# Optimization experiments

Hardware: AMD Instinct MI355X
Metric: run time of the kernel (lower is better)

The kernel has to match this reference:

```python
import jax, jax.numpy as jnp
import numpy as np

B, T, D_MODEL, H, W = 2, 3, 32, 256, 256
N_HEADS, N_LEVELS, N_POINTS = 4, 3, 4


def conv2d(x, w, b, padding=1, dilation=1):
    y = jax.lax.conv_general_dilated(
        x, w, window_strides=(1, 1),
        padding=[(padding, padding), (padding, padding)],
        rhs_dilation=(dilation, dilation),
        dimension_numbers=('NCHW', 'OIHW', 'NCHW'))
    return y + b[None, :, None, None]


def lrelu(x):
    return jnp.where(x >= 0, x, 0.1 * x)


def bilinear_sample(img, x, y):
    # img: (N,C,H,W); x,y: (N,H',W') pixel coords; zero padding outside (grid_sample zeros)
    N, C, Hh, Ww = img.shape
    x0 = jnp.floor(x); y0 = jnp.floor(y)
    lx = x - x0; ly = y - y0
    imf = img.reshape(N, C, Hh * Ww)
    out = jnp.zeros((N, C) + x.shape[1:], img.dtype)
    for dy, dx, wgt in ((0, 0, (1 - lx) * (1 - ly)), (0, 1, lx * (1 - ly)),
                        (1, 0, (1 - lx) * ly), (1, 1, lx * ly)):
        xi = x0 + dx; yi = y0 + dy
        valid = (xi >= 0) & (xi < Ww) & (yi >= 0) & (yi < Hh)
        idx = (jnp.clip(yi, 0, Hh - 1) * Ww + jnp.clip(xi, 0, Ww - 1)).astype(jnp.int32)
        g = jnp.take_along_axis(imf, idx.reshape(N, 1, -1), axis=2).reshape((N, C) + x.shape[1:])
        out = out + g * (wgt * valid)[:, None]
    return out


def flow_warp(x, flow):
    # torch flow_warp with align_corners=True == sampling at pixel coords grid+flow
    N, C, Hh, Ww = x.shape
    gy, gx = jnp.meshgrid(jnp.arange(Hh, dtype=x.dtype), jnp.arange(Ww, dtype=x.dtype), indexing='ij')
    return bilinear_sample(x, gx[None] + flow[:, 0], gy[None] + flow[:, 1])


def ms_deform_attn(value, sampling_locations, attention_weights, h, w):
    # value: (N, L*h*w, Hh, d); loc: (N, Lq, Hh, L, P, 2) in [0,1]; weights: (N, Lq, Hh, L, P)
    # Matches MSDA CUDA kernel: sample at loc*(W,H)-0.5, bilinear, zero pad outside.
    N, _, Hh, d = value.shape
    Lq = sampling_locations.shape[1]
    L, P = sampling_locations.shape[3], sampling_locations.shape[4]
    out = jnp.zeros((N, Lq, Hh, d), value.dtype)
    for l in range(L):
        v = value[:, l * h * w:(l + 1) * h * w].transpose(0, 2, 1, 3)  # (N,Hh,hw,d)
        loc = sampling_locations[:, :, :, l]  # (N,Lq,Hh,P,2)
        x = loc[..., 0] * w - 0.5
        y = loc[..., 1] * h - 0.5
        x0 = jnp.floor(x); y0 = jnp.floor(y)
        lx = x - x0; ly = y - y0
        samp = jnp.zeros((N, Lq, Hh, P, d), value.dtype)
        for dy, dx, wgt in ((0, 0, (1 - lx) * (1 - ly)), (0, 1, lx * (1 - ly)),
                            (1, 0, (1 - lx) * ly), (1, 1, lx * ly)):
            xi = x0 + dx; yi = y0 + dy
            valid = (xi >= 0) & (xi < w) & (yi >= 0) & (yi < h)
            idx = (jnp.clip(yi, 0, h - 1) * w + jnp.clip(xi, 0, w - 1)).astype(jnp.int32)
            idx = idx.transpose(0, 2, 1, 3).reshape(N, Hh, Lq * P)
            g = jnp.take_along_axis(v, idx[..., None], axis=2)  # (N,Hh,Lq*P,d)
            g = g.reshape(N, Hh, Lq, P, d).transpose(0, 2, 1, 3, 4)
            samp = samp + g * (wgt * valid)[..., None]
        out = out + (samp * attention_weights[:, :, :, l][..., None]).sum(axis=3)
    return out.reshape(N, Lq, Hh * d)


def setup_inputs() -> dict:
    key = jax.random.key(0)
    ks = jax.random.split(key, 24)
    def rn(k, shape, s=1.0):
        return jax.random.normal(k, shape, dtype=jnp.float32) * s
    c = D_MODEL
    nofp = N_HEADS * N_LEVELS * N_POINTS
    return {
        'frame': rn(ks[0], (B, T, c, H, W)),
        'srcframe': rn(ks[1], (B, T, c, H, W)),
        'flow_forward': rn(ks[2], (B, T - 1, 2, H, W), 2.0),
        'flow_backward': rn(ks[3], (B, T - 1, 2, H, W), 2.0),
        'W_qk': rn(ks[4], (3 * c, 3 * c + 4, 3, 3), 0.05), 'b_qk': rn(ks[5], (3 * c,), 0.05),
        'W_v': rn(ks[6], (3 * c, 3 * c, 3, 3), 0.05), 'b_v': rn(ks[7], (3 * c,), 0.05),
        'W_vp': rn(ks[8], (c, c, 3, 3), 0.05), 'b_vp': rn(ks[9], (c,), 0.05),
        'W_off': rn(ks[10], (nofp * 2, 3 * c, 3, 3), 0.01), 'b_off': rn(ks[11], (nofp * 2,), 0.5),
        'W_aw': rn(ks[12], (nofp, 3 * c, 3, 3), 0.05), 'b_aw': rn(ks[13], (nofp,), 0.05),
        'W_out': rn(ks[14], (c, c, 3, 3), 0.05), 'b_out': rn(ks[15], (c,), 0.05),
        'W_ffd': rn(ks[16], (c, c, 3, 3), 0.05), 'b_ffd': rn(ks[17], (c,), 0.05),
        'W_ff1': rn(ks[18], (c, 2 * c, 3, 3), 0.05), 'b_ff1': rn(ks[19], (c,), 0.05),
        'W_ff2': rn(ks[20], (c, c, 3, 3), 0.05), 'b_ff2': rn(ks[21], (c,), 0.05),
        'W_fu': rn(ks[22], (c, c, 1, 1), 0.05), 'b_fu': rn(ks[23], (c,), 0.05),
    }


def reference(frame, srcframe, flow_forward, flow_backward,
              W_qk, b_qk, W_v, b_v, W_vp, b_vp, W_off, b_off, W_aw, b_aw,
              W_out, b_out, W_ffd, b_ffd, W_ff1, b_ff1, W_ff2, b_ff2, W_fu, b_fu):
    b, t, c, h, w = frame.shape
    Hh, L, P = N_HEADS, N_LEVELS, N_POINTS
    d = c // Hh
    # flow-warped neighbor frames + flows -> query embedding
    warp01 = flow_warp(frame[:, 0], flow_backward[:, 0])
    warp21 = flow_warp(frame[:, 2], flow_forward[:, 1])
    qk_in = jnp.concatenate([warp01, frame[:, 1], warp21,
                             flow_forward[:, 1], flow_backward[:, 0]], axis=1)
    qureys = lrelu(conv2d(qk_in, W_qk, b_qk))                       # (b, 3c, h, w)
    value = conv2d(frame.reshape(b, t * c, h, w), W_v, b_v)         # (b, 3c, h, w)
    # --- MSDeformAttn_Fusion ---
    val = conv2d(value.reshape(b * t, c, h, w), W_vp, b_vp).reshape(b, t, c, h, w)
    off = conv2d(qureys, W_off, b_off)                               # (b, Hh*L*P*2, h, w)
    aw = conv2d(qureys, W_aw, b_aw)                                  # (b, Hh*L*P, h, w)
    value_flat = val.reshape(b, t, c, h * w).transpose(0, 1, 3, 2).reshape(b, t * h * w, Hh, d)
    off = off.reshape(b, -1, h * w).transpose(0, 2, 1).reshape(b, h * w, Hh, L, P, 2)
    aw = aw.reshape(b, -1, h * w).transpose(0, 2, 1).reshape(b, h * w, Hh, L * P)
    aw = jax.nn.softmax(aw, axis=-1).reshape(b, h * w, Hh, L, P)
    # reference points: pixel centers normalized (masks all zero -> valid_ratios == 1)
    gy, gx = jnp.meshgrid((jnp.arange(h, dtype=off.dtype) + 0.5) / h,
                          (jnp.arange(w, dtype=off.dtype) + 0.5) / w, indexing='ij')
    ref = jnp.stack([gx.reshape(-1), gy.reshape(-1)], -1)            # (hw, 2) (x, y)
    normalizer = jnp.array([w, h], dtype=off.dtype)                  # same for all levels
    loc = ref[None, :, None, None, None, :] + off / normalizer
    attn_out = ms_deform_attn(value_flat, loc, aw, h, w)             # (b, hw, c)
    out = attn_out.reshape(b, h, w, c).transpose(0, 3, 1, 2)
    out = conv2d(out, W_out, b_out)                                  # output_proj
    # --- post-attention ---
    out = conv2d(out, W_ffd, b_ffd) + frame[:, 1]
    tseq = jnp.concatenate([out, srcframe[:, 1]], axis=1)            # (b, 2c, h, w)
    ff = conv2d(lrelu(conv2d(tseq, W_ff1, b_ff1, padding=2, dilation=2)), W_ff2, b_ff2)
    out = out + ff
    out = lrelu(conv2d(out, W_fu, b_fu, padding=0))                  # fusion 1x1
    return out
```

## Files before the change

### kernel.cpp

```cpp
#include <hip/hip_runtime.h>
#include <hip/hip_bf16.h>

typedef __hip_bfloat16 bf16;
typedef unsigned short us;
typedef __attribute__((ext_vector_type(8))) short short8;
typedef __attribute__((ext_vector_type(8))) unsigned short ushortx8;
typedef __attribute__((ext_vector_type(4))) float f32x4;

#define HW 65536
#define IMW 256
#define IMH 256

static __device__ __forceinline__ float u2f(us u) {
  return __uint_as_float(((unsigned)u) << 16);
}
static __device__ __forceinline__ us f2bu(float x) {
  bf16 h = __float2bfloat16(x);
  return *reinterpret_cast<us*>(&h);
}
static __device__ __forceinline__ unsigned pk2(float a, float b) {
  return (unsigned)f2bu(a) | ((unsigned)f2bu(b) << 16);
}

struct PrepArgs {
  const float* src[9];
  us* dst[9];
  int OC[9], CIN[9], KPAD[9];
};

__global__ __launch_bounds__(256) void prep_weights(PrepArgs a) {
  int j = blockIdx.y;
  int n = blockIdx.x * 256 + threadIdx.x;
  int OC = a.OC[j], CIN = a.CIN[j], KPAD = a.KPAD[j];
  int tot = 9 * OC * KPAD;
  if (n >= tot) return;
  int t = n / (OC * KPAD);
  int rem = n - t * OC * KPAD;
  int oc = rem / KPAD;
  int k = rem - oc * KPAD;
  float v = (k < CIN) ? a.src[j][(size_t)(oc * CIN + k) * 9 + t] : 0.f;
  a.dst[j][n] = f2bu(v);
}

__global__ __launch_bounds__(256) void frame_to_nhwc(const float* __restrict__ frame,
                                                     unsigned* __restrict__ fn) {
  int pix = blockIdx.x * 256 + threadIdx.x;
  int b = blockIdx.y;
  const float* s = frame + (size_t)b * 96 * HW + pix;
  unsigned u[48];
#pragma unroll
  for (int j = 0; j < 48; ++j)
    u[j] = pk2(s[(size_t)(2 * j) * HW], s[(size_t)(2 * j + 1) * HW]);
  unsigned* d = fn + ((size_t)b * HW + pix) * 48;
#pragma unroll
  for (int j = 0; j < 12; ++j) {
    uint4 w;
    w.x = u[4 * j]; w.y = u[4 * j + 1]; w.z = u[4 * j + 2]; w.w = u[4 * j + 3];
    *(uint4*)&d[4 * j] = w;
  }
}

static __device__ void warp_nhwc(const us* __restrict__ fn, size_t bbase, int coff,
                                 float x, float y, unsigned* uo) {
  float x0f = floorf(x), y0f = floorf(y);
  float lx = x - x0f, ly = y - y0f;
  int x0 = (int)x0f, y0 = (int)y0f;
  float wt[4] = {(1.f - lx) * (1.f - ly), lx * (1.f - ly), (1.f - lx) * ly, lx * ly};
  float acc[32] = {};
#pragma unroll
  for (int k = 0; k < 4; ++k) {
    int xi = x0 + (k & 1), yi = y0 + (k >> 1);
    if ((unsigned)xi < IMW && (unsigned)yi < IMH) {
      const ushortx8* s =
          (const ushortx8*)(fn + (bbase + (size_t)yi * IMW + xi) * 96 + coff);
      float w = wt[k];
#pragma unroll
      for (int cj = 0; cj < 4; ++cj) {
        ushortx8 vv = s[cj];
#pragma unroll
        for (int e = 0; e < 8; ++e)
          acc[cj * 8 + e] = fmaf(w, u2f(vv[e]), acc[cj * 8 + e]);
      }
    }
  }
#pragma unroll
  for (int j = 0; j < 16; ++j) uo[j] = pk2(acc[2 * j], acc[2 * j + 1]);
}

__global__ __launch_bounds__(256) void build_qkin(
    const us* __restrict__ fn, const float* __restrict__ flowf,
    const float* __restrict__ flowb, unsigned* __restrict__ qk) {
  int pix = blockIdx.x * 256 + threadIdx.x;
  int b = blockIdx.y;
  int px = pix & 255, py = pix >> 8;

  float fbx = flowb[((size_t)(b * 2 + 0) * 2 + 0) * HW + pix];
  float fby = flowb[((size_t)(b * 2 + 0) * 2 + 1) * HW + pix];
  float ffx = flowf[((size_t)(b * 2 + 1) * 2 + 0) * HW + pix];
  float ffy = flowf[((size_t)(b * 2 + 1) * 2 + 1) * HW + pix];

  unsigned u[50];
  {
    const unsigned* s = (const unsigned*)(fn + ((size_t)b * HW + pix) * 96);
#pragma unroll
    for (int j = 0; j < 16; ++j) u[16 + j] = s[16 + j];
  }
  u[48] = pk2(ffx, ffy);
  u[49] = pk2(fbx, fby);

  warp_nhwc(fn, (size_t)b * HW, 0, (float)px + fbx, (float)py + fby, &u[0]);
  warp_nhwc(fn, (size_t)b * HW, 64, (float)px + ffx, (float)py + ffy, &u[32]);

  unsigned* qb = qk + ((size_t)b * HW + pix) * 50;
#pragma unroll
  for (int j = 0; j < 25; ++j) {
    uint2 t;
    t.x = u[2 * j];
    t.y = u[2 * j + 1];
    *(uint2*)(qb + 2 * j) = t;
  }
}

template <int CIN, int CST, int KPAD, int KCH, int DIL, int G, int ZDIV, int CSUB,
          int RES, int OUTMODE, bool LRELU>
__global__ __launch_bounds__(256) void conv3x3_mfma(
    const us* __restrict__ in, const us* __restrict__ W2,
    const float* __restrict__ bias, void* __restrict__ out, int out_cst,
    int out_coff, float* __restrict__ outB, const float* __restrict__ res,
    int res_cst, int res_coff) {
  constexpr int OC = G * 16;
  constexpr int COLS = 16 + 2 * DIL;
  constexpr int ROWS = 8 + 2 * DIL;
  constexpr int HALO = ROWS * COLS;
  constexpr int CIPAD = KCH + 8;
  constexpr int CH = KCH / 8;
  constexpr int NST = KPAD / KCH;
  constexpr int GW0 = (G + 1) / 2;
  __shared__ alignas(16) short lds[HALO * CIPAD];

  const int z = blockIdx.z;
  const int bin = z / ZDIV;
  const int coff = (z % ZDIV) * CSUB;
  const int px0 = blockIdx.x * 16, py0 = blockIdx.y * 8;
  const int lane = threadIdx.x & 63;
  const int wv = threadIdx.x >> 6;
  const int m = lane & 15, q = lane >> 4;
  const int gh = wv & 1, rh = wv >> 1;
  const int goff = gh * GW0;

  f32x4 acc[GW0][4];
#pragma unroll
  for (int g = 0; g < GW0; ++g)
#pragma unroll
    for (int r = 0; r < 4; ++r) acc[g][r] = 0.f;

#pragma unroll 1
  for (int s = 0; s < NST; ++s) {
    for (int c = threadIdx.x; c < HALO * CH; c += 256) {
      int p = c / CH, cb = c - p * CH;
      int row = p / COLS, col = p - row * COLS;
      int gy = py0 + row - DIL, gx = px0 + col - DIL;
      bool ok = ((unsigned)gy < IMH) && ((unsigned)gx < IMW);
      int ci0 = s * KCH + cb * 8;
      const us* gp = in + ((size_t)bin * HW + (size_t)gy * IMW + gx) * CST + coff + ci0;
      if (CIN == KPAD) {
        short8 v = (short8)0;
        if (ok) v = *(const short8*)gp;
        *(short8*)&lds[p * CIPAD + cb * 8] = v;
      } else {
        uint2 h0; h0.x = 0; h0.y = 0;
        uint2 h1; h1.x = 0; h1.y = 0;
        if (ok && ci0 + 4 <= CIN) h0 = *(const uint2*)gp;
        if (ok && ci0 + 8 <= CIN) h1 = *(const uint2*)(gp + 4);
        *(uint2*)&lds[p * CIPAD + cb * 8] = h0;
        *(uint2*)&lds[p * CIPAD + cb * 8 + 4] = h1;
      }
    }
    __syncthreads();

#pragma unroll
    for (int t = 0; t < 9; ++t) {
      const int dy = t / 3 - 1, dx = t - (t / 3) * 3 - 1;
#pragma unroll
      for (int kc = 0; kc < KCH / 32; ++kc) {
        short8 bfr[4];
#pragma unroll
        for (int r = 0; r < 4; ++r) {
          int rr = rh * 4 + r + DIL + dy * DIL;
          int cc = m + DIL + dx * DIL;
          bfr[r] = *(const short8*)&lds[(rr * COLS + cc) * CIPAD + kc * 32 + q * 8];
        }
#pragma unroll
        for (int g = 0; g < GW0; ++g) {
          if (goff + g < G) {
            short8 af = *(const short8*)(W2 +
                (size_t)(t * OC + (goff + g) * 16 + m) * KPAD + s * KCH + kc * 32 + q * 8);
#pragma unroll
            for (int r = 0; r < 4; ++r)
              acc[g][r] =
                  __builtin_amdgcn_mfma_f32_16x16x32_bf16(af, bfr[r], acc[g][r], 0, 0, 0);
          }
        }
      }
    }
    if (s + 1 < NST) __syncthreads();
  }

#pragma unroll
  for (int g = 0; g < GW0; ++g) {
    if (goff + g < G) {
      int oc0 = (goff + g) * 16 + q * 4;
      f32x4 bb = *(const f32x4*)&bias[oc0];
#pragma unroll
      for (int r = 0; r < 4; ++r) {
        int py = py0 + rh * 4 + r;
        int px = px0 + m;
        size_t pix = (size_t)py * IMW + px;
        f32x4 v;
#pragma unroll
        for (int e = 0; e < 4; ++e) {
          float x = acc[g][r][e] + bb[e];
          if (LRELU) x = x >= 0.f ? x : 0.1f * x;
          v[e] = x;
        }
        if (RES == 1) {
          f32x4 rv = *(const f32x4*)&res[((size_t)z * HW + pix) * res_cst + oc0];
#pragma unroll
          for (int e = 0; e < 4; ++e) v[e] += rv[e];
        }
        if (RES == 2) {
#pragma unroll
          for (int e = 0; e < 4; ++e)
            v[e] += res[((size_t)z * res_cst + res_coff + oc0 + e) * HW + pix];
        }
        if (OUTMODE == 0 || OUTMODE == 3) {
          uint2 w;
          w.x = pk2(v[0], v[1]);
          w.y = pk2(v[2], v[3]);
          *(uint2*)&((us*)out)[((size_t)z * HW + pix) * out_cst + out_coff + oc0] = w;
        }
        if (OUTMODE == 2)
          *(f32x4*)&((float*)out)[((size_t)z * HW + pix) * out_cst + oc0] = v;
        if (OUTMODE == 3)
          *(f32x4*)&outB[((size_t)z * HW + pix) * 32 + oc0] = v;
      }
    }
  }
}

__global__ __launch_bounds__(256) void deform_attn(
    const us* __restrict__ valp, const us* __restrict__ off,
    const float* __restrict__ aw, us* __restrict__ outp) {
  int tid = threadIdx.x;
  int hh = tid & 3;
  int pix = blockIdx.x * 64 + (tid >> 2);
  int b = blockIdx.y;
  int px = pix & (IMW - 1), py = pix >> 8;
  float refx = ((float)px + 0.5f) * (1.0f / IMW);
  float refy = ((float)py + 0.5f) * (1.0f / IMH);

  ushortx8 o8[3];
  {
    const ushortx8* ob =
        (const ushortx8*)(off + ((size_t)b * HW + pix) * 96 + hh * 24);
#pragma unroll
    for (int j = 0; j < 3; ++j) o8[j] = ob[j];
  }
  f32x4 a4[3];
  {
    const f32x4* ab = (const f32x4*)(aw + ((size_t)b * HW + pix) * 48 + hh * 12);
#pragma unroll
    for (int j = 0; j < 3; ++j) a4[j] = ab[j];
  }

  float wv[12];
  float mx = -1e30f;
#pragma unroll
  for (int lp = 0; lp < 12; ++lp) {
    wv[lp] = a4[lp >> 2][lp & 3];
    mx = fmaxf(mx, wv[lp]);
  }
  float s = 0.f;
#pragma unroll
  for (int lp = 0; lp < 12; ++lp) {
    wv[lp] = __expf(wv[lp] - mx);
    s += wv[lp];
  }
  float inv = 1.f / s;

  float acc[8] = {0.f, 0.f, 0.f, 0.f, 0.f, 0.f, 0.f, 0.f};
#pragma unroll 1
  for (int l = 0; l < 3; ++l) {
    const us* vbase = valp + ((size_t)(b * 3 + l) * HW) * 32 + hh * 8;
#pragma unroll
    for (int p = 0; p < 4; ++p) {
      int ch = l * 8 + p * 2;
      float ox = u2f(o8[ch >> 3][ch & 7]);
      float oy = u2f(o8[(ch + 1) >> 3][(ch + 1) & 7]);
      float x = (refx + ox * (1.0f / IMW)) * (float)IMW - 0.5f;
      float y = (refy + oy * (1.0f / IMH)) * (float)IMH - 0.5f;
      float x0f = floorf(x), y0f = floorf(y);
      float lx = x - x0f, ly = y - y0f;
      int x0 = (int)x0f, y0 = (int)y0f;
      float a = wv[l * 4 + p] * inv;
      float cw[4] = {(1.f - lx) * (1.f - ly) * a, lx * (1.f - ly) * a,
                     (1.f - lx) * ly * a, lx * ly * a};
#pragma unroll
      for (int k = 0; k < 4; ++k) {
        int xi = x0 + (k & 1), yi = y0 + (k >> 1);
        if ((unsigned)xi < IMW && (unsigned)yi < IMH) {
          const ushortx8 u = *(const ushortx8*)(vbase + (size_t)(yi * IMW + xi) * 32);
          float wgt = cw[k];
#pragma unroll
          for (int dd = 0; dd < 8; ++dd) acc[dd] = fmaf(wgt, u2f(u[dd]), acc[dd]);
        }
      }
    }
  }
  ushortx8 sv;
#pragma unroll
  for (int dd = 0; dd < 8; ++dd) sv[dd] = f2bu(acc[dd]);
  *(ushortx8*)(outp + ((size_t)b * HW + pix) * 32 + hh * 8) = sv;
}

__global__ __launch_bounds__(256) void copy_src(const float* __restrict__ src,
                                                unsigned* __restrict__ out1b) {
  int pix = blockIdx.x * 256 + threadIdx.x;
  int b = blockIdx.y;
  const float* s = src + ((size_t)(b * 3 + 1) * 32) * HW + pix;
  unsigned u[16];
#pragma unroll
  for (int j = 0; j < 16; ++j)
    u[j] = pk2(s[(size_t)(2 * j) * HW], s[(size_t)(2 * j + 1) * HW]);
  unsigned* d = out1b + ((size_t)b * HW + pix) * 32 + 16;
#pragma unroll
  for (int j = 0; j < 4; ++j) {
    uint4 w;
    w.x = u[4 * j]; w.y = u[4 * j + 1]; w.z = u[4 * j + 2]; w.w = u[4 * j + 3];
    *(uint4*)&d[4 * j] = w;
  }
}

__global__ __launch_bounds__(256) void conv1x1_fu(
    const float* __restrict__ in, const float* __restrict__ wgt,
    const float* __restrict__ bias, float* __restrict__ out) {
  int pix = blockIdx.x * 256 + threadIdx.x;
  int b = blockIdx.y;
  float vin[32];
  {
    const f32x4* s = (const f32x4*)(in + ((size_t)b * HW + pix) * 32);
#pragma unroll
    for (int j = 0; j < 8; ++j) {
      f32x4 v = s[j];
#pragma unroll
      for (int e = 0; e < 4; ++e) vin[4 * j + e] = v[e];
    }
  }
#pragma unroll 1
  for (int oc = 0; oc < 32; ++oc) {
    float a = bias[oc];
#pragma unroll
    for (int ci = 0; ci < 32; ++ci) a = fmaf(wgt[oc * 32 + ci], vin[ci], a);
    a = a >= 0.f ? a : 0.1f * a;
    out[((size_t)b * 32 + oc) * HW + pix] = a;
  }
}

extern "C" void kernel_launch(void* const* d_in, const int* in_sizes, int n_in,
                              void* d_out, int out_size, void* d_ws, size_t ws_size,
                              hipStream_t stream) {
  (void)in_sizes; (void)n_in; (void)out_size;
  if (ws_size < 25614592ull * 4) return;

  const float* frame = (const float*)d_in[0];
  const float* srcframe = (const float*)d_in[1];
  const float* flowf = (const float*)d_in[2];
  const float* flowb = (const float*)d_in[3];

  float* ws = (float*)d_ws;
  us* wsu = (us*)d_ws;

  static const int w2off[9] = {0,      110592, 193536, 202752, 285696,
                               327168, 336384, 345600, 364032};
  us* fnhwc = (us*)(ws + 186624);
  unsigned* qk_u = (unsigned*)(ws + 6478080);
  us* qk = (us*)qk_u;
  us* Q = (us*)(ws + 13031680);
  us* V = (us*)(ws + 6478080);
  us* Vp = (us*)(ws + 19323136);
  us* offb = (us*)(ws + 186624);
  float* awb = (float*)(ws + 6478080);
  us* attn = (us*)(ws + 13031680);
  us* convout = (us*)(ws + 13031680 + 2097152);
  us* out1b = (us*)(ws + 6478080);
  unsigned* out1b_u = (unsigned*)out1b;
  float* out1f = (float*)(ws + 19323136);
  us* ff1out = (us*)(ws + 186624);
  float* out2 = (float*)(ws + 13031680);

  {
    PrepArgs pa;
    static const int srcidx[9] = {4, 6, 8, 10, 12, 14, 16, 18, 20};
    static const int OCs[9] = {96, 96, 32, 96, 48, 32, 32, 32, 32};
    static const int CINs[9] = {100, 96, 32, 96, 96, 32, 32, 64, 32};
    static const int KPADs[9] = {128, 96, 32, 96, 96, 32, 32, 64, 32};
    for (int i = 0; i < 9; ++i) {
      pa.src[i] = (const float*)d_in[srcidx[i]];
      pa.dst[i] = wsu + w2off[i];
      pa.OC[i] = OCs[i];
      pa.CIN[i] = CINs[i];
      pa.KPAD[i] = KPADs[i];
    }
    prep_weights<<<dim3(432, 9), 256, 0, stream>>>(pa);
  }

  frame_to_nhwc<<<dim3(256, 2), 256, 0, stream>>>(frame, (unsigned*)fnhwc);

  build_qkin<<<dim3(256, 2), 256, 0, stream>>>(fnhwc, flowf, flowb, qk_u);

  dim3 cg2(16, 32, 2);

  conv3x3_mfma<100, 100, 128, 64, 1, 6, 1, 0, 0, 0, true><<<cg2, 256, 0, stream>>>(
      qk, wsu + w2off[0], (const float*)d_in[5], Q, 96, 0, nullptr, nullptr, 0, 0);

  conv3x3_mfma<96, 96, 96, 32, 1, 6, 1, 0, 0, 0, false><<<cg2, 256, 0, stream>>>(
      fnhwc, wsu + w2off[1], (const float*)d_in[7], V, 96, 0, nullptr, nullptr, 0, 0);

  conv3x3_mfma<32, 96, 32, 32, 1, 2, 3, 32, 0, 0, false><<<dim3(16, 32, 6), 256, 0, stream>>>(
      V, wsu + w2off[2], (const float*)d_in[9], Vp, 32, 0, nullptr, nullptr, 0, 0);

  conv3x3_mfma<96, 96, 96, 32, 1, 6, 1, 0, 0, 0, false><<<cg2, 256, 0, stream>>>(
      Q, wsu + w2off[3], (const float*)d_in[11], offb, 96, 0, nullptr, nullptr, 0, 0);

  conv3x3_mfma<96, 96, 96, 32, 1, 3, 1, 0, 0, 2, false><<<cg2, 256, 0, stream>>>(
      Q, wsu + w2off[4], (const float*)d_in[13], awb, 48, 0, nullptr, nullptr, 0, 0);

  deform_attn<<<dim3(1024, 2), 256, 0, stream>>>(Vp, offb, awb, attn);

  conv3x3_mfma<32, 32, 32, 32, 1, 2, 1, 0, 0, 0, false><<<cg2, 256, 0, stream>>>(
      attn, wsu + w2off[5], (const float*)d_in[15], convout, 32, 0, nullptr, nullptr, 0, 0);

  conv3x3_mfma<32, 32, 32, 32, 1, 2, 1, 0, 2, 3, false><<<cg2, 256, 0, stream>>>(
      convout, wsu + w2off[6], (const float*)d_in[17], out1b, 64, 0, out1f, frame, 96, 32);

  copy_src<<<dim3(256, 2), 256, 0, stream>>>(srcframe, out1b_u);

  conv3x3_mfma<64, 64, 64, 32, 2, 2, 1, 0, 0, 0, true><<<cg2, 256, 0, stream>>>(
      out1b, wsu + w2off[7], (const float*)d_in[19], ff1out, 32, 0, nullptr, nullptr, 0, 0);

  conv3x3_mfma<32, 32, 32, 32, 1, 2, 1, 0, 1, 2, false><<<cg2, 256, 0, stream>>>(
      ff1out, wsu + w2off[8], (const float*)d_in[21], out2, 32, 0, nullptr, out1f, 32, 0);

  conv1x1_fu<<<dim3(256, 2), 256, 0, stream>>>(out2, (const float*)d_in[22],
                                               (const float*)d_in[23], (float*)d_out);
}
```

Before: 524.0 us.

## Pre-swizzle conv weights into MFMA fragment order, load full-K halo once, prefetch weights

The weight-prep kernel now writes bf16 weights in a fragment-major layout, so each lane fetches its MFMA A-operand with one contiguous 16-byte load at lane*8. The conv kernel drops the K-chunk staging loop and loads the whole channel depth of the halo into LDS in a single pass with one barrier. It then iterates over (tap, k-chunk) units, double-buffering the weight fragments in registers so the next unit's loads overlap the current MFMAs. Launch bounds now request 4 blocks per CU. The trade-off is larger LDS use for wide-channel layers (KPAD=128), which may limit occupancy, plus more register pressure from the prefetched fragments.

```diff
diff --git a/kernel.cpp b/kernel.cpp
--- a/kernel.cpp
+++ b/kernel.cpp
@@ -34,10 +34,17 @@
   int OC = a.OC[j], CIN = a.CIN[j], KPAD = a.KPAD[j];
   int tot = 9 * OC * KPAD;
   if (n >= tot) return;
-  int t = n / (OC * KPAD);
-  int rem = n - t * OC * KPAD;
-  int oc = rem / KPAD;
-  int k = rem - oc * KPAD;
+  int G = OC >> 4, NKC = KPAD >> 5;
+  int e = n & 7;
+  int m = (n >> 3) & 15;
+  int q = (n >> 7) & 3;
+  int rest = n >> 9;
+  int kc = rest % NKC;
+  int tg = rest / NKC;
+  int g = tg % G;
+  int t = tg / G;
+  int oc = g * 16 + m;
+  int k = kc * 32 + q * 8 + e;
   float v = (k < CIN) ? a.src[j][(size_t)(oc * CIN + k) * 9 + t] : 0.f;
   a.dst[j][n] = f2bu(v);
 }
@@ -121,9 +128,9 @@
   }
 }
 
-template <int CIN, int CST, int KPAD, int KCH, int DIL, int G, int ZDIV, int CSUB,
+template <int CIN, int CST, int KPAD, int DIL, int G, int ZDIV, int CSUB,
           int RES, int OUTMODE, bool LRELU>
-__global__ __launch_bounds__(256) void conv3x3_mfma(
+__global__ __launch_bounds__(256, 4) void conv3x3_mfma(
     const us* __restrict__ in, const us* __restrict__ W2,
     const float* __restrict__ bias, void* __restrict__ out, int out_cst,
     int out_coff, float* __restrict__ outB, const float* __restrict__ res,
@@ -132,10 +139,11 @@
   constexpr int COLS = 16 + 2 * DIL;
   constexpr int ROWS = 8 + 2 * DIL;
   constexpr int HALO = ROWS * COLS;
-  constexpr int CIPAD = KCH + 8;
-  constexpr int CH = KCH / 8;
-  constexpr int NST = KPAD / KCH;
+  constexpr int CIPAD = KPAD + 8;
+  constexpr int CH = KPAD / 8;
+  constexpr int NKC = KPAD / 32;
   constexpr int GW0 = (G + 1) / 2;
+  constexpr int NU = 9 * NKC;
   __shared__ alignas(16) short lds[HALO * CIPAD];
 
   const int z = blockIdx.z;
@@ -154,56 +162,69 @@
 #pragma unroll
     for (int r = 0; r < 4; ++r) acc[g][r] = 0.f;
 
-#pragma unroll 1
-  for (int s = 0; s < NST; ++s) {
-    for (int c = threadIdx.x; c < HALO * CH; c += 256) {
-      int p = c / CH, cb = c - p * CH;
+  {
+    int p = threadIdx.x;
+    if (p < HALO) {
       int row = p / COLS, col = p - row * COLS;
       int gy = py0 + row - DIL, gx = px0 + col - DIL;
       bool ok = ((unsigned)gy < IMH) && ((unsigned)gx < IMW);
-      int ci0 = s * KCH + cb * 8;
-      const us* gp = in + ((size_t)bin * HW + (size_t)gy * IMW + gx) * CST + coff + ci0;
+      const us* gp = in + ((size_t)bin * HW + (size_t)gy * IMW + gx) * CST + coff;
       if (CIN == KPAD) {
-        short8 v = (short8)0;
-        if (ok) v = *(const short8*)gp;
-        *(short8*)&lds[p * CIPAD + cb * 8] = v;
+#pragma unroll
+        for (int cb = 0; cb < CH; ++cb) {
+          short8 v = (short8)0;
+          if (ok) v = *(const short8*)(gp + cb * 8);
+          *(short8*)&lds[p * CIPAD + cb * 8] = v;
+        }
       } else {
-        uint2 h0; h0.x = 0; h0.y = 0;
-        uint2 h1; h1.x = 0; h1.y = 0;
-        if (ok && ci0 + 4 <= CIN) h0 = *(const uint2*)gp;
-        if (ok && ci0 + 8 <= CIN) h1 = *(const uint2*)(gp + 4);
-        *(uint2*)&lds[p * CIPAD + cb * 8] = h0;
-        *(uint2*)&lds[p * CIPAD + cb * 8 + 4] = h1;
+#pragma unroll
+        for (int cb = 0; cb < CH; ++cb) {
+          uint2 h0; h0.x = 0; h0.y = 0;
+          uint2 h1; h1.x = 0; h1.y = 0;
+          int ci0 = cb * 8;
+          if (ok && ci0 + 4 <= CIN) h0 = *(const uint2*)(gp + ci0);
+          if (ok && ci0 + 8 <= CIN) h1 = *(const uint2*)(gp + ci0 + 4);
+          *(uint2*)&lds[p * CIPAD + ci0] = h0;
+          *(uint2*)&lds[p * CIPAD + ci0 + 4] = h1;
+        }
       }
     }
-    __syncthreads();
-
-#pragma unroll
-    for (int t = 0; t < 9; ++t) {
-      const int dy = t / 3 - 1, dx = t - (t / 3) * 3 - 1;
-#pragma unroll
-      for (int kc = 0; kc < KCH / 32; ++kc) {
-        short8 bfr[4];
-#pragma unroll
-        for (int r = 0; r < 4; ++r) {
-          int rr = rh * 4 + r + DIL + dy * DIL;
-          int cc = m + DIL + dx * DIL;
-          bfr[r] = *(const short8*)&lds[(rr * COLS + cc) * CIPAD + kc * 32 + q * 8];
-        }
-#pragma unroll
-        for (int g = 0; g < GW0; ++g) {
-          if (goff + g < G) {
-            short8 af = *(const short8*)(W2 +
-                (size_t)(t * OC + (goff + g) * 16 + m) * KPAD + s * KCH + kc * 32 + q * 8);
-#pragma unroll
-            for (int r = 0; r < 4; ++r)
-              acc[g][r] =
-                  __builtin_amdgcn_mfma_f32_16x16x32_bf16(af, bfr[r], acc[g][r], 0, 0, 0);
-          }
-        }
-      }
-    }
-    if (s + 1 < NST) __syncthreads();
+  }
+  __syncthreads();
+
+  const us* wl = W2 + (size_t)lane * 8;
+  short8 af[2][GW0];
+#pragma unroll
+  for (int g = 0; g < GW0; ++g)
+    if (goff + g < G)
+      af[0][g] = *(const short8*)(wl + (size_t)((goff + g) * NKC) * 512);
+
+#pragma unroll
+  for (int u = 0; u < NU; ++u) {
+    const int t = u / NKC, kc = u - t * NKC;
+    if (u + 1 < NU) {
+      const int t1 = (u + 1) / NKC, kc1 = (u + 1) - t1 * NKC;
+#pragma unroll
+      for (int g = 0; g < GW0; ++g)
+        if (goff + g < G)
+          af[(u + 1) & 1][g] =
+              *(const short8*)(wl + (size_t)((t1 * G + goff + g) * NKC + kc1) * 512);
+    }
+    const int dy = t / 3 - 1, dx = t - (t / 3) * 3 - 1;
+    short8 bfr[4];
+#pragma unroll
+    for (int r = 0; r < 4; ++r) {
+      int rr = rh * 4 + r + DIL + dy * DIL;
+      int cc = m + DIL + dx * DIL;
+      bfr[r] = *(const short8*)&lds[(rr * COLS + cc) * CIPAD + kc * 32 + q * 8];
+    }
+#pragma unroll
+    for (int g = 0; g < GW0; ++g)
+      if (goff + g < G)
+#pragma unroll
+        for (int r = 0; r < 4; ++r)
+          acc[g][r] = __builtin_amdgcn_mfma_f32_16x16x32_bf16(af[u & 1][g], bfr[r],
+                                                              acc[g][r], 0, 0, 0);
   }
 
 #pragma unroll
@@ -420,35 +441,35 @@
 
   dim3 cg2(16, 32, 2);
 
-  conv3x3_mfma<100, 100, 128, 64, 1, 6, 1, 0, 0, 0, true><<<cg2, 256, 0, stream>>>(
+  conv3x3_mfma<100, 100, 128, 1, 6, 1, 0, 0, 0, true><<<cg2, 256, 0, stream>>>(
       qk, wsu + w2off[0], (const float*)d_in[5], Q, 96, 0, nullptr, nullptr, 0, 0);
 
-  conv3x3_mfma<96, 96, 96, 32, 1, 6, 1, 0, 0, 0, false><<<cg2, 256, 0, stream>>>(
+  conv3x3_mfma<96, 96, 96, 1, 6, 1, 0, 0, 0, false><<<cg2, 256, 0, stream>>>(
       fnhwc, wsu + w2off[1], (const float*)d_in[7], V, 96, 0, nullptr, nullptr, 0, 0);
 
-  conv3x3_mfma<32, 96, 32, 32, 1, 2, 3, 32, 0, 0, false><<<dim3(16, 32, 6), 256, 0, stream>>>(
+  conv3x3_mfma<32, 96, 32, 1, 2, 3, 32, 0, 0, false><<<dim3(16, 32, 6), 256, 0, stream>>>(
       V, wsu + w2off[2], (const float*)d_in[9], Vp, 32, 0, nullptr, nullptr, 0, 0);
 
-  conv3x3_mfma<96, 96, 96, 32, 1, 6, 1, 0, 0, 0, false><<<cg2, 256, 0, stream>>>(
+  conv3x3_mfma<96, 96, 96, 1, 6, 1, 0, 0, 0, false><<<cg2, 256, 0, stream>>>(
       Q, wsu + w2off[3], (const float*)d_in[11], offb, 96, 0, nullptr, nullptr, 0, 0);
 
-  conv3x3_mfma<96, 96, 96, 32, 1, 3, 1, 0, 0, 2, false><<<cg2, 256, 0, stream>>>(
+  conv3x3_mfma<96, 96, 96, 1, 3, 1, 0, 0, 2, false><<<cg2, 256, 0, stream>>>(
       Q, wsu + w2off[4], (const float*)d_in[13], awb, 48, 0, nullptr, nullptr, 0, 0);
 
   deform_attn<<<dim3(1024, 2), 256, 0, stream>>>(Vp, offb, awb, attn);
 
-  conv3x3_mfma<32, 32, 32, 32, 1, 2, 1, 0, 0, 0, false><<<cg2, 256, 0, stream>>>(
+  conv3x3_mfma<32, 32, 32, 1, 2, 1, 0, 0, 0, false><<<cg2, 256, 0, stream>>>(
       attn, wsu + w2off[5], (const float*)d_in[15], convout, 32, 0, nullptr, nullptr, 0, 0);
 
-  conv3x3_mfma<32, 32, 32, 32, 1, 2, 1, 0, 2, 3, false><<<cg2, 256, 0, stream>>>(
+  conv3x3_mfma<32, 32, 32, 1, 2, 1, 0, 2, 3, false><<<cg2, 256, 0, stream>>>(
       convout, wsu + w2off[6], (const float*)d_in[17], out1b, 64, 0, out1f, frame, 96, 32);
 
   copy_src<<<dim3(256, 2), 256, 0, stream>>>(srcframe, out1b_u);
 
-  conv3x3_mfma<64, 64, 64, 32, 2, 2, 1, 0, 0, 0, true><<<cg2, 256, 0, stream>>>(
+  conv3x3_mfma<64, 64, 64, 2, 2, 1, 0, 0, 0, true><<<cg2, 256, 0, stream>>>(
       out1b, wsu + w2off[7], (const float*)d_in[19], ff1out, 32, 0, nullptr, nullptr, 0, 0);
 
-  conv3x3_mfma<32, 32, 32, 32, 1, 2, 1, 0, 1, 2, false><<<cg2, 256, 0, stream>>>(
+  conv3x3_mfma<32, 32, 32, 1, 2, 1, 0, 1, 2, false><<<cg2, 256, 0, stream>>>(
       ff1out, wsu + w2off[8], (const float*)d_in[21], out2, 32, 0, nullptr, out1f, 32, 0);
 
   conv1x1_fu<<<dim3(256, 2), 256, 0, stream>>>(out2, (const float*)d_in[22],
```

After: 589.7 us. 1.13x slower.
